# Optimization experiments

Hardware: AMD Instinct MI355X
Metric: run time of the kernel (lower is better)

## Reference

```python
import jax, jax.numpy as jnp
import numpy as np

B, S, H, NH = 2, 2048, 4096, 32
D = H // NH  # head_dim = 128
ROPE_THETA = 10000.0


def setup_inputs() -> dict:
    key = jax.random.key(0)
    k0, k1, k2 = jax.random.split(key, 3)
    hidden_states = jax.random.normal(k0, (B, S, H), dtype=jnp.float32) * 0.02
    w_pack = jax.random.normal(k1, (H, 3 * H), dtype=jnp.float32) * 0.02  # fused QKV weight
    w_o = jax.random.normal(k2, (H, H), dtype=jnp.float32) * 0.02         # o_proj weight
    positions = jnp.broadcast_to(jnp.arange(S, dtype=jnp.int32), (B, S))
    return {"positions": positions, "hidden_states": hidden_states, "w_pack": w_pack, "w_o": w_o}


def _rope(x, positions):
    # neox-style rotary embedding (vLLM get_rope default), x: [B, S, NH, D]
    half = D // 2
    inv_freq = 1.0 / (ROPE_THETA ** (jnp.arange(0, half, dtype=jnp.float32) * 2.0 / D))
    freqs = positions.astype(jnp.float32)[..., None] * inv_freq  # [B, S, half]
    cos = jnp.cos(freqs)[:, :, None, :]  # [B, S, 1, half]
    sin = jnp.sin(freqs)[:, :, None, :]
    x1, x2 = x[..., :half], x[..., half:]
    return jnp.concatenate([x1 * cos - x2 * sin, x2 * cos + x1 * sin], axis=-1)


def reference(positions, hidden_states, w_pack, w_o):
    # fused QKV projection
    qkv = jnp.einsum('bsh,hf->bsf', hidden_states, w_pack)
    q, k, v = jnp.split(qkv, 3, axis=-1)
    q = q.reshape(B, S, NH, D)
    k = k.reshape(B, S, NH, D)
    v = v.reshape(B, S, NH, D)
    # RoPE on q, k
    q = _rope(q, positions)
    k = _rope(k, positions)
    # causal scaled dot-product attention
    scale = D ** -0.5
    scores = jnp.einsum('bqhd,bkhd->bhqk', q, k) * scale  # [B, NH, S, S]
    causal = jnp.tril(jnp.ones((S, S), dtype=bool))
    scores = jnp.where(causal[None, None], scores, jnp.finfo(scores.dtype).min)
    probs = jax.nn.softmax(scores, axis=-1)
    out = jnp.einsum('bhqk,bkhd->bqhd', probs, v).reshape(B, S, H)
    # output projection
    return jnp.einsum('bsh,hf->bsf', out, w_o)
```

## Files before the change

kernel.cpp:

```cpp
#include <hip/hip_runtime.h>

#define Sdim   2048
#define Hdim   4096
#define NHEADS 32
#define Dh     128
#define Mrows  4096
#define QKVLD  12288

typedef __attribute__((ext_vector_type(8))) short short8;
typedef __attribute__((ext_vector_type(4))) float f32x4;
typedef __attribute__((ext_vector_type(4))) float float4v;

__device__ __forceinline__ short f2bf(float f) {
  union { float f; unsigned u; } x; x.f = f;
  unsigned r = x.u + 0x7fffu + ((x.u >> 16) & 1u);
  return (short)(r >> 16);
}
__device__ __forceinline__ float bf2f(short s) {
  union { unsigned u; float f; } x; x.u = ((unsigned)(unsigned short)s) << 16;
  return x.f;
}

__device__ __forceinline__ void gload_lds16(const void* g, void* l) {
  __builtin_amdgcn_global_load_lds(
      (const __attribute__((address_space(1))) void*)g,
      (__attribute__((address_space(3))) void*)l, 16, 0, 0);
}

__global__ void k_cvt(const float* __restrict__ src, short* __restrict__ dst, int n8) {
  int idx = blockIdx.x * blockDim.x + threadIdx.x;
  if (idx >= n8) return;
  const float4v* s = (const float4v*)src + (size_t)idx * 2;
  float4v a = s[0], b = s[1];
  short8 o;
  o[0] = f2bf(a.x); o[1] = f2bf(a.y); o[2] = f2bf(a.z); o[3] = f2bf(a.w);
  o[4] = f2bf(b.x); o[5] = f2bf(b.y); o[6] = f2bf(b.z); o[7] = f2bf(b.w);
  *((short8*)dst + idx) = o;
}

__global__ void k_tcvt64(const float* __restrict__ src, short* __restrict__ dst,
                         int R, int C) {
  __shared__ float t[64][65];
  const int tid = threadIdx.x;
  const int r0 = blockIdx.y * 64, c0 = blockIdx.x * 64;
  const int ir = tid >> 4, ic = (tid & 15) << 2;
#pragma unroll
  for (int p = 0; p < 4; ++p) {
    const float4v v = *(const float4v*)(src + (size_t)(r0 + p * 16 + ir) * C + c0 + ic);
    t[p * 16 + ir][ic] = v.x; t[p * 16 + ir][ic + 1] = v.y;
    t[p * 16 + ir][ic + 2] = v.z; t[p * 16 + ir][ic + 3] = v.w;
  }
  __syncthreads();
  const int oc = tid >> 3, orr = (tid & 7) << 3;
#pragma unroll
  for (int p = 0; p < 2; ++p) {
    int c = p * 32 + oc;
    short8 o;
#pragma unroll
    for (int j = 0; j < 8; ++j) o[j] = f2bf(t[orr + j][c]);
    *(short8*)(dst + (size_t)(c0 + c) * R + r0 + orr) = o;
  }
}

__global__ void k_vt64(const short* __restrict__ qkv, short* __restrict__ vt) {
  __shared__ short tile[4096];
  const int tid = threadIdx.x;
  const int c0 = blockIdx.x * 64;
  const int s0 = blockIdx.y * 64;
  const int b  = blockIdx.z;
#pragma unroll
  for (int j = 0; j < 2; ++j) {
    int chunk = j * 256 + tid;
    int row = chunk >> 3, c8 = chunk & 7;
    short8 v = *(const short8*)(qkv + (size_t)(b * 2048 + s0 + row) * QKVLD + 8192 + c0 + c8 * 8);
    int sw = c8 ^ ((row ^ (row >> 3)) & 7);
    *(short8*)((char*)tile + row * 128 + sw * 16) = v;
  }
  __syncthreads();
#pragma unroll
  for (int j = 0; j < 2; ++j) {
    int chunk = j * 256 + tid;
    int d = chunk >> 3, s8 = (chunk & 7) << 3;
    short8 o;
#pragma unroll
    for (int j2 = 0; j2 < 8; ++j2) {
      int s = s8 + j2;
      int sw = ((d >> 3) ^ ((s ^ (s >> 3)) & 7));
      o[j2] = *(const short*)((const char*)tile + s * 128 + sw * 16 + (d & 7) * 2);
    }
    *(short8*)(vt + (size_t)(b * 4096 + c0 + d) * Sdim + s0 + s8) = o;
  }
}

__device__ __forceinline__ void stage_half256(const short* G, int ld, int row0, int kcol,
                                              char* lds, int tid) {
#pragma unroll
  for (int j = 0; j < 2; ++j) {
    int p = j * 512 + tid;
    int r = p >> 3;
    int c = ((p & 7) ^ (r & 7)) << 3;
    gload_lds16(G + (size_t)(row0 + r) * ld + kcol + c,
                lds + ((j * 512 + (tid & 448)) << 4));
  }
}

#define MFMA_Q(qm, qn)                                                                   \
  do {                                                                                   \
    __builtin_amdgcn_s_setprio(1);                                                       \
    _Pragma("unroll")                                                                    \
    for (int m4 = 0; m4 < 4; ++m4)                                                       \
      _Pragma("unroll")                                                                  \
      for (int n2 = 0; n2 < 2; ++n2) {                                                   \
        acc[(qm)*4+m4][(qn)*2+n2] = __builtin_amdgcn_mfma_f32_16x16x32_bf16(             \
            av[m4][0], bv[(qn)*2+n2][0], acc[(qm)*4+m4][(qn)*2+n2], 0, 0, 0);            \
        acc[(qm)*4+m4][(qn)*2+n2] = __builtin_amdgcn_mfma_f32_16x16x32_bf16(             \
            av[m4][1], bv[(qn)*2+n2][1], acc[(qm)*4+m4][(qn)*2+n2], 0, 0, 0);            \
      }                                                                                  \
    __builtin_amdgcn_s_setprio(0);                                                       \
  } while (0)

#define PH_BARRIER()                    \
  do {                                  \
    __builtin_amdgcn_s_barrier();       \
    __builtin_amdgcn_sched_barrier(0);  \
  } while (0)

template<bool C_F32>
__global__ __launch_bounds__(512, 2) void k_gemm256(const short* __restrict__ A, int lda,
                                                    const short* __restrict__ Bt, int ldb,
                                                    void* __restrict__ Cp, int ldc,
                                                    int Ndim, int Kdim) {
  __shared__ __align__(16) char smem[131072];
  const int tid  = threadIdx.x;
  const int lane = tid & 63;
  const int wave = tid >> 6;
  const int lo = lane & 15, hi = lane >> 4;
  const int wr = wave >> 2, wc = wave & 3;

  const int nblk = gridDim.x;
  const int lid = (blockIdx.x & 7) * (nblk >> 3) + (blockIdx.x >> 3);
  const int nbn = Ndim >> 8;
  const int bm0 = (lid / nbn) << 8;
  const int bn0 = (lid % nbn) << 8;

  f32x4 acc[8][4];
#pragma unroll
  for (int i = 0; i < 8; ++i)
#pragma unroll
    for (int j = 0; j < 4; ++j) acc[i][j] = (f32x4){0.f, 0.f, 0.f, 0.f};

  short8 av[4][2], bv[4][2];
  const int swz = (lo & 7) << 4;
  const int brow = (wc & 1) * 64;

  stage_half256(Bt, ldb, bn0,       0, smem + 32768,         tid);
  stage_half256(Bt, ldb, bn0 + 128, 0, smem + 32768 + 16384, tid);
  stage_half256(A,  lda, bm0,       0, smem,                 tid);
  stage_half256(A,  lda, bm0 + 128, 0, smem + 16384,         tid);

  const int NK = Kdim >> 6;
  for (int kt = 0; kt < NK; ++kt) {
    const int cur = kt & 1;
    const char* Ab = smem + cur * 65536 + wr * 16384;
    const char* Bb = smem + cur * 65536 + 32768 + (wc >> 1) * 16384;
    char* nA = smem + (cur ^ 1) * 65536;
    char* nB = nA + 32768;
    const int kc = (kt + 1) << 6;
    const bool pf = (kt + 1 < NK);

    if (pf) {
      stage_half256(Bt, ldb, bn0,       kc, nB,         tid);
      stage_half256(Bt, ldb, bn0 + 128, kc, nB + 16384, tid);
      asm volatile("s_waitcnt vmcnt(4)" ::: "memory");
    } else {
      asm volatile("s_waitcnt vmcnt(0)" ::: "memory");
    }
    PH_BARRIER();
#pragma unroll
    for (int m4 = 0; m4 < 4; ++m4)
#pragma unroll
      for (int ks = 0; ks < 2; ++ks)
        av[m4][ks] = *(const short8*)(Ab + (m4 * 16 + lo) * 128 + ((ks * 64 + hi * 16) ^ swz));
#pragma unroll
    for (int ni = 0; ni < 2; ++ni)
#pragma unroll
      for (int ks = 0; ks < 2; ++ks)
        bv[ni][ks] = *(const short8*)(Bb + (brow + ni * 16 + lo) * 128 + ((ks * 64 + hi * 16) ^ swz));
    MFMA_Q(0, 0);
#pragma unroll
    for (int ni = 2; ni < 4; ++ni)
#pragma unroll
      for (int ks = 0; ks < 2; ++ks)
        bv[ni][ks] = *(const short8*)(Bb + (brow + ni * 16 + lo) * 128 + ((ks * 64 + hi * 16) ^ swz));

    if (pf) {
      stage_half256(A, lda, bm0,       kc, nA,         tid);
      stage_half256(A, lda, bm0 + 128, kc, nA + 16384, tid);
    }
    PH_BARRIER();
    MFMA_Q(0, 1);
#pragma unroll
    for (int m4 = 0; m4 < 4; ++m4)
#pragma unroll
      for (int ks = 0; ks < 2; ++ks)
        av[m4][ks] = *(const short8*)(Ab + ((64 + m4 * 16 + lo) * 128) + ((ks * 64 + hi * 16) ^ swz));

    PH_BARRIER();
    MFMA_Q(1, 0);

    PH_BARRIER();
    MFMA_Q(1, 1);
  }

#pragma unroll
  for (int mi = 0; mi < 8; ++mi)
#pragma unroll
    for (int r = 0; r < 4; ++r) {
      int row = bm0 + wr * 128 + mi * 16 + hi * 4 + r;
#pragma unroll
      for (int ni = 0; ni < 4; ++ni) {
        int col = bn0 + wc * 64 + ni * 16 + lo;
        if (C_F32) ((float*)Cp)[(size_t)row * ldc + col] = acc[mi][ni][r];
        else       ((short*)Cp)[(size_t)row * ldc + col] = f2bf(acc[mi][ni][r]);
      }
    }
}

__global__ void k_rope8(short* qkv, const int* __restrict__ positions) {
  int idx = blockIdx.x * 256 + threadIdx.x;
  int t = idx & 7;
  int h = (idx >> 3) & 31;
  int row = idx >> 8;
  float pos = (float)positions[row];
  size_t o = (size_t)row * QKVLD + h * 128 + t * 8;
  short8 q1 = *(short8*)(qkv + o),        q2 = *(short8*)(qkv + o + 64);
  short8 k1 = *(short8*)(qkv + o + 4096), k2 = *(short8*)(qkv + o + 4160);
#pragma unroll
  for (int j = 0; j < 8; ++j) {
    int d = t * 8 + j;
    float inv = exp2f((float)d * -0.2076205059304570f);
    float ang = pos * inv, s, c;
    sincosf(ang, &s, &c);
    float a1 = bf2f(q1[j]), a2 = bf2f(q2[j]);
    q1[j] = f2bf(a1 * c - a2 * s); q2[j] = f2bf(a2 * c + a1 * s);
    float b1 = bf2f(k1[j]), b2 = bf2f(k2[j]);
    k1[j] = f2bf(b1 * c - b2 * s); k2[j] = f2bf(b2 * c + b1 * s);
  }
  *(short8*)(qkv + o) = q1;        *(short8*)(qkv + o + 64) = q2;
  *(short8*)(qkv + o + 4096) = k1; *(short8*)(qkv + o + 4160) = k2;
}

__device__ __forceinline__ void stage_kv(const short* Kb, const short* Vtb, int kv0,
                                         char* kbuf, char* vbuf, int tid, int wave) {
#pragma unroll
  for (int i = 0; i < 4; ++i) {
    int p = i * 256 + tid;
    int r = p >> 4;
    int c = (p & 15) ^ (r & 7);
    gload_lds16(Kb + (size_t)(kv0 + r) * QKVLD + (c << 3),
                kbuf + ((i * 256 + wave * 64) << 4));
  }
#pragma unroll
  for (int i = 0; i < 4; ++i) {
    int p = i * 256 + tid;
    int r = p >> 3;
    int c = (p & 7) ^ (r & 7);
    gload_lds16(Vtb + (size_t)r * Sdim + kv0 + (c << 3),
                vbuf + ((i * 256 + wave * 64) << 4));
  }
}

__global__ __launch_bounds__(256, 2) void k_attn(short* __restrict__ qkv,
                                                 const short* __restrict__ Vt) {
  __shared__ __align__(16) char smem[81920];
  const int tid  = threadIdx.x;
  const int lane = tid & 63;
  const int wave = tid >> 6;
  const int lo = lane & 15, hi = lane >> 4;

  const int bid = blockIdx.x;
  const int lid = (bid & 7) * 128 + (bid >> 3);
  const int bh = lid >> 4;
  const int qt = 15 - (lid & 15);
  const int b = bh >> 5, h = bh & 31;
  const int q0 = qt << 7;

  short* base = qkv + (size_t)b * Sdim * QKVLD;
  const short* Qb = base + h * Dh;
  const short* Kb = base + Hdim + h * Dh;
  const short* Vtb = Vt + (size_t)(b * 32 + h) * 128 * Sdim;
  const int qrow0 = q0 + wave * 32;

  short* Pw = (short*)(smem + 65536 + wave * 4096);

  short8 qf[2][4];
#pragma unroll
  for (int mi = 0; mi < 2; ++mi)
#pragma unroll
    for (int ks = 0; ks < 4; ++ks)
      qf[mi][ks] = *(const short8*)(Qb + (size_t)(qrow0 + mi * 16 + lo) * QKVLD + ks * 32 + hi * 8);

  f32x4 acc_o[2][9];
  float m_run[2][4];
#pragma unroll
  for (int mi = 0; mi < 2; ++mi) {
#pragma unroll
    for (int nf = 0; nf < 9; ++nf) acc_o[mi][nf] = (f32x4){0.f, 0.f, 0.f, 0.f};
#pragma unroll
    for (int r = 0; r < 4; ++r) m_run[mi][r] = -1e30f;
  }

  short8 vones;
#pragma unroll
  for (int j = 0; j < 8; ++j) vones[j] = (short)0x3F80;

  const float SEXP = 0.088388347648318447f * 1.4426950408889634f;
  const int nkv = (q0 + 128) >> 6;
  const int swz = (lo & 7) << 4;

  stage_kv(Kb, Vtb, 0, smem, smem + 16384, tid, wave);
  __syncthreads();

  int cur = 0;
  for (int kvt = 0; kvt < nkv; ++kvt) {
    const int kv0 = kvt << 6;
    if (kvt + 1 < nkv)
      stage_kv(Kb, Vtb, kv0 + 64, smem + (cur ^ 1) * 32768,
               smem + (cur ^ 1) * 32768 + 16384, tid, wave);

    if (kv0 <= qrow0 + 31) {
      const char* kl = smem + cur * 32768;
      const char* vl = smem + cur * 32768 + 16384;

      f32x4 accs[2][4];
#pragma unroll
      for (int mi = 0; mi < 2; ++mi)
#pragma unroll
        for (int nf = 0; nf < 4; ++nf) accs[mi][nf] = (f32x4){0.f, 0.f, 0.f, 0.f};
#pragma unroll
      for (int ks = 0; ks < 4; ++ks) {
        short8 kf[4];
#pragma unroll
        for (int nf = 0; nf < 4; ++nf) {
          int r = nf * 16 + lo;
          kf[nf] = *(const short8*)(kl + r * 256 + ((ks * 64 + hi * 16) ^ swz));
        }
        __builtin_amdgcn_s_setprio(1);
#pragma unroll
        for (int mi = 0; mi < 2; ++mi)
#pragma unroll
          for (int nf = 0; nf < 4; ++nf)
            accs[mi][nf] = __builtin_amdgcn_mfma_f32_16x16x32_bf16(qf[mi][ks], kf[nf], accs[mi][nf], 0, 0, 0);
        __builtin_amdgcn_s_setprio(0);
      }

      const bool needmask = (kv0 + 63 > qrow0);
      float pmax[2][4];
      bool okall = true;
#pragma unroll
      for (int mi = 0; mi < 2; ++mi) {
#pragma unroll
        for (int r = 0; r < 4; ++r) {
          const int qrow = qrow0 + mi * 16 + hi * 4 + r;
          float tmax = -1e30f;
#pragma unroll
          for (int nf = 0; nf < 4; ++nf) {
            float v = accs[mi][nf][r] * SEXP;
            if (needmask) {
              int col = kv0 + nf * 16 + lo;
              v = (col <= qrow) ? v : -1e30f;
            }
            accs[mi][nf][r] = v;
            tmax = fmaxf(tmax, v);
          }
#pragma unroll
          for (int off = 1; off < 16; off <<= 1)
            tmax = fmaxf(tmax, __shfl_xor(tmax, off, 64));
          pmax[mi][r] = tmax;
          okall = okall && (tmax <= m_run[mi][r] + 8.0f);
        }
      }
      if (!__all(okall)) {
#pragma unroll
        for (int mi = 0; mi < 2; ++mi)
#pragma unroll
          for (int r = 0; r < 4; ++r) {
            float mnew = fmaxf(m_run[mi][r], pmax[mi][r]);
            float alpha = exp2f(m_run[mi][r] - mnew);
            m_run[mi][r] = mnew;
#pragma unroll
            for (int nf = 0; nf < 9; ++nf) acc_o[mi][nf][r] *= alpha;
          }
      }
#pragma unroll
      for (int mi = 0; mi < 2; ++mi)
#pragma unroll
        for (int r = 0; r < 4; ++r) {
          const int prow = mi * 16 + hi * 4 + r;
          const int psw = prow & 7;
#pragma unroll
          for (int nf = 0; nf < 4; ++nf) {
            float p = exp2f(accs[mi][nf][r] - m_run[mi][r]);
            int col = nf * 16 + lo;
            Pw[(prow << 6) + (((col >> 3) ^ psw) << 3) + (col & 7)] = f2bf(p);
          }
        }

#pragma unroll
      for (int ks = 0; ks < 2; ++ks) {
        short8 pf[2];
#pragma unroll
        for (int mi = 0; mi < 2; ++mi) {
          int prow = mi * 16 + lo;
          pf[mi] = *(const short8*)((const char*)Pw + prow * 128 + (((ks * 4 + hi) ^ (prow & 7)) << 4));
        }
        __builtin_amdgcn_s_setprio(1);
#pragma unroll
        for (int nf = 0; nf < 9; ++nf) {
          short8 vf;
          if (nf < 8) {
            int row = nf * 16 + lo;
            vf = *(const short8*)(vl + row * 128 + ((ks * 64 + hi * 16) ^ swz));
          } else {
            vf = vones;
          }
#pragma unroll
          for (int mi = 0; mi < 2; ++mi)
            acc_o[mi][nf] = __builtin_amdgcn_mfma_f32_16x16x32_bf16(pf[mi], vf, acc_o[mi][nf], 0, 0, 0);
        }
        __builtin_amdgcn_s_setprio(0);
      }
    }

    __syncthreads();
    cur ^= 1;
  }

  short* Osm = (short*)smem;
#pragma unroll
  for (int mi = 0; mi < 2; ++mi)
#pragma unroll
    for (int r = 0; r < 4; ++r) {
      float inv = 1.0f / acc_o[mi][8][r];
      int row = wave * 32 + mi * 16 + hi * 4 + r;
#pragma unroll
      for (int nf = 0; nf < 8; ++nf)
        Osm[row * 128 + nf * 16 + lo] = f2bf(acc_o[mi][nf][r] * inv);
    }
  __syncthreads();
  short* Ob = base + h * Dh;
#pragma unroll
  for (int it = 0; it < 8; ++it) {
    int chunk = it * 256 + tid;
    int row = chunk >> 4, c8 = chunk & 15;
    *(short8*)(Ob + (size_t)(q0 + row) * QKVLD + c8 * 8) =
        *(const short8*)(Osm + row * 128 + c8 * 8);
  }
}

extern "C" void kernel_launch(void* const* d_in, const int* in_sizes, int n_in,
                              void* d_out, int out_size, void* d_ws, size_t ws_size,
                              hipStream_t stream) {
  const int*   positions = (const int*)d_in[0];
  const float* hidden    = (const float*)d_in[1];
  const float* w_pack    = (const float*)d_in[2];
  const float* w_o       = (const float*)d_in[3];
  float* out = (float*)d_out;

  char* ws = (char*)d_ws;
  short* Wpt  = (short*)ws;
  short* qkvb = (short*)(ws + (size_t)12288 * 4096 * 2);
  short* Wot  = (short*)ws;
  short* Hbf  = (short*)d_out;
  short* Vtg  = (short*)((char*)d_out + ((size_t)32 << 20));

  k_cvt<<<8192, 256, 0, stream>>>(hidden, Hbf, 4096 * 4096 / 8);
  k_tcvt64<<<dim3(12288 / 64, 4096 / 64), 256, 0, stream>>>(w_pack, Wpt, 4096, 12288);
  k_gemm256<false><<<dim3(768), 512, 0, stream>>>(Hbf, 4096, Wpt, 4096, qkvb, QKVLD, 12288, 4096);
  k_rope8<<<4096, 256, 0, stream>>>(qkvb, positions);
  k_vt64<<<dim3(64, 32, 2), 256, 0, stream>>>(qkvb, Vtg);
  k_attn<<<dim3(1024), 256, 0, stream>>>(qkvb, Vtg);
  k_tcvt64<<<dim3(4096 / 64, 4096 / 64), 256, 0, stream>>>(w_o, Wot, 4096, 4096);
  k_gemm256<true><<<dim3(256), 512, 0, stream>>>(qkvb, QKVLD, Wot, 4096, out, 4096, 4096, 4096);
}
```

Before: 760.2 us.

## Simplify GEMM and attention pipelines to one barrier per K/KV iteration

The GEMM main loop drops its four phase barriers and split A/B prefetch. Each iteration now waits for all loads and hits one barrier, then issues the whole next-tile prefetch at once. The attention loop likewise swaps its trailing __syncthreads for a single waitcnt plus barrier at the top of each iteration. This cuts synchronisation overhead but loses the staggered load/MFMA interleaving and the ping-pong phasing across waves. Removing the trailing barrier may also race the prefetch into the buffer other waves are still reading.

After: 789.9 us. 3.9% more time.

```diff
diff --git a/kernel.cpp b/kernel.cpp
--- a/kernel.cpp
+++ b/kernel.cpp
@@ -119,12 +119,6 @@
     __builtin_amdgcn_s_setprio(0);                                                       \
   } while (0)
 
-#define PH_BARRIER()                    \
-  do {                                  \
-    __builtin_amdgcn_s_barrier();       \
-    __builtin_amdgcn_sched_barrier(0);  \
-  } while (0)
-
 template<bool C_F32>
 __global__ __launch_bounds__(512, 2) void k_gemm256(const short* __restrict__ A, int lda,
                                                     const short* __restrict__ Bt, int ldb,
@@ -153,29 +147,30 @@
   const int swz = (lo & 7) << 4;
   const int brow = (wc & 1) * 64;
 
+  stage_half256(A,  lda, bm0,       0, smem,                 tid);
+  stage_half256(A,  lda, bm0 + 128, 0, smem + 16384,         tid);
   stage_half256(Bt, ldb, bn0,       0, smem + 32768,         tid);
   stage_half256(Bt, ldb, bn0 + 128, 0, smem + 32768 + 16384, tid);
-  stage_half256(A,  lda, bm0,       0, smem,                 tid);
-  stage_half256(A,  lda, bm0 + 128, 0, smem + 16384,         tid);
 
   const int NK = Kdim >> 6;
   for (int kt = 0; kt < NK; ++kt) {
     const int cur = kt & 1;
     const char* Ab = smem + cur * 65536 + wr * 16384;
     const char* Bb = smem + cur * 65536 + 32768 + (wc >> 1) * 16384;
-    char* nA = smem + (cur ^ 1) * 65536;
-    char* nB = nA + 32768;
-    const int kc = (kt + 1) << 6;
-    const bool pf = (kt + 1 < NK);
-
-    if (pf) {
-      stage_half256(Bt, ldb, bn0,       kc, nB,         tid);
-      stage_half256(Bt, ldb, bn0 + 128, kc, nB + 16384, tid);
-      asm volatile("s_waitcnt vmcnt(4)" ::: "memory");
-    } else {
-      asm volatile("s_waitcnt vmcnt(0)" ::: "memory");
+
+    asm volatile("s_waitcnt vmcnt(0)" ::: "memory");
+    __builtin_amdgcn_s_barrier();
+    __builtin_amdgcn_sched_barrier(0);
+
+    if (kt + 1 < NK) {
+      char* nS = smem + ((cur ^ 1) * 65536);
+      const int kc = (kt + 1) << 6;
+      stage_half256(A,  lda, bm0,       kc, nS,         tid);
+      stage_half256(A,  lda, bm0 + 128, kc, nS + 16384, tid);
+      stage_half256(Bt, ldb, bn0,       kc, nS + 32768, tid);
+      stage_half256(Bt, ldb, bn0 + 128, kc, nS + 49152, tid);
     }
-    PH_BARRIER();
+
 #pragma unroll
     for (int m4 = 0; m4 < 4; ++m4)
 #pragma unroll
@@ -192,23 +187,13 @@
 #pragma unroll
       for (int ks = 0; ks < 2; ++ks)
         bv[ni][ks] = *(const short8*)(Bb + (brow + ni * 16 + lo) * 128 + ((ks * 64 + hi * 16) ^ swz));
-
-    if (pf) {
-      stage_half256(A, lda, bm0,       kc, nA,         tid);
-      stage_half256(A, lda, bm0 + 128, kc, nA + 16384, tid);
-    }
-    PH_BARRIER();
     MFMA_Q(0, 1);
 #pragma unroll
     for (int m4 = 0; m4 < 4; ++m4)
 #pragma unroll
       for (int ks = 0; ks < 2; ++ks)
         av[m4][ks] = *(const short8*)(Ab + ((64 + m4 * 16 + lo) * 128) + ((ks * 64 + hi * 16) ^ swz));
-
-    PH_BARRIER();
     MFMA_Q(1, 0);
-
-    PH_BARRIER();
     MFMA_Q(1, 1);
   }
 
@@ -319,11 +304,14 @@
   const int swz = (lo & 7) << 4;
 
   stage_kv(Kb, Vtb, 0, smem, smem + 16384, tid, wave);
-  __syncthreads();
 
   int cur = 0;
   for (int kvt = 0; kvt < nkv; ++kvt) {
     const int kv0 = kvt << 6;
+
+    asm volatile("s_waitcnt vmcnt(0)" ::: "memory");
+    __builtin_amdgcn_s_barrier();
+    __builtin_amdgcn_sched_barrier(0);
     if (kvt + 1 < nkv)
       stage_kv(Kb, Vtb, kv0 + 64, smem + (cur ^ 1) * 32768,
                smem + (cur ^ 1) * 32768 + 16384, tid, wave);
@@ -432,10 +420,10 @@
       }
     }
 
-    __syncthreads();
     cur ^= 1;
   }
 
+  __syncthreads();
   short* Osm = (short*)smem;
 #pragma unroll
   for (int mi = 0; mi < 2; ++mi)
```
